# Kernel optimization log

Hardware: AMD Instinct MI355X
Metric: run time of the kernel (lower is better)

## Reference

```python
import jax, jax.numpy as jnp
import numpy as np

HID = 2048 * 3  # infl_ratio = 3
EPS = 1e-5
P_DROP = 0.5


def sign_ste(x):
    # straight-through binarization: sign in fwd, identity in bwd
    return x + jax.lax.stop_gradient(jnp.sign(x) - x)


def batchnorm(x, g, b):
    # training-mode BatchNorm1d: batch stats, biased variance
    m = jnp.mean(x, axis=0)
    v = jnp.mean((x - m) ** 2, axis=0)
    return g * (x - m) / jnp.sqrt(v + EPS) + b


def hardtanh(x):
    return jnp.clip(x, -1.0, 1.0)


def dropout(x, u):
    # u ~ U[0,1); keep where u >= p, scale by 1/(1-p)
    return jnp.where(u >= P_DROP, x / (1.0 - P_DROP), 0.0)


def setup_inputs() -> dict:
    key = jax.random.key(0)
    ks = jax.random.split(key, 16)
    B = 512
    d = {}
    d['x'] = jax.random.normal(ks[0], (B, 784), dtype=jnp.float32)
    d['drop_mask_bin'] = jax.random.uniform(ks[1], (B, HID), dtype=jnp.float32)
    d['drop_mask_real'] = jax.random.uniform(ks[2], (B, HID), dtype=jnp.float32)
    s1 = 1.0 / np.sqrt(784)
    sh = 1.0 / np.sqrt(HID)
    d['w1'] = jax.random.uniform(ks[3], (HID, 784), jnp.float32, -s1, s1)
    d['b1'] = jax.random.uniform(ks[4], (HID,), jnp.float32, -s1, s1)
    d['w2'] = jax.random.uniform(ks[5], (HID, HID), jnp.float32, -sh, sh)
    d['b2'] = jax.random.uniform(ks[6], (HID,), jnp.float32, -sh, sh)
    d['w3'] = jax.random.uniform(ks[7], (HID, HID), jnp.float32, -sh, sh)
    d['b3'] = jax.random.uniform(ks[8], (HID,), jnp.float32, -sh, sh)
    d['w4'] = jax.random.uniform(ks[9], (10, HID), jnp.float32, -sh, sh)
    d['b4'] = jax.random.uniform(ks[10], (10,), jnp.float32, -sh, sh)
    for i, k in zip((1, 2, 3), (ks[11], ks[12], ks[13])):
        d[f'g{i}'] = jnp.ones((HID,), jnp.float32)
        d[f'be{i}'] = jnp.zeros((HID,), jnp.float32)
    return d


def reference(x, drop_mask_bin, drop_mask_real, w1, b1, w2, b2, w3, b3, w4, b4,
              g1, be1, g2, be2, g3, be3):
    sg = jax.lax.stop_gradient
    # layer 1: input dim 784 -> input NOT binarized; weights binarized
    Bout1 = x @ sign_ste(w1).T + b1
    Rout1 = sg(x @ w1.T + b1)
    Bout1 = hardtanh(batchnorm(Bout1, g1, be1))
    Rout1 = sg(hardtanh(batchnorm(Rout1, g1, be1)))
    # layer 2: binarize activations and weights on binary path
    Bout2 = sign_ste(Bout1) @ sign_ste(w2).T + b2
    Rout2 = sg(Rout1 @ w2.T + b2)
    Bout2 = hardtanh(batchnorm(Bout2, g2, be2))
    Rout2 = sg(hardtanh(batchnorm(Rout2, g2, be2)))
    # layer 3 + dropout
    Bout3 = sign_ste(Bout2) @ sign_ste(w3).T + b3
    Rout3 = sg(Rout2 @ w3.T + b3)
    Bout3 = hardtanh(batchnorm(dropout(Bout3, drop_mask_bin), g3, be3))
    Rout3 = sg(hardtanh(batchnorm(dropout(Rout3, drop_mask_real), g3, be3)))
    # classifier (real-valued Linear)
    out = Bout3 @ w4.T + b4
    logp = jax.nn.log_softmax(out, axis=1)
    return (logp, out, Bout1, Rout1, Bout2, Rout2, Bout3, Rout3)
```

## Files before the change

kernel.cpp:

```cpp
#include <hip/hip_runtime.h>


typedef _Float16 f16x8 __attribute__((ext_vector_type(8)));
typedef _Float16 f16x4 __attribute__((ext_vector_type(4)));
typedef float f32x4 __attribute__((ext_vector_type(4)));
typedef int i32x4 __attribute__((ext_vector_type(4)));

#define MFMA16(a, b, c) __builtin_amdgcn_mfma_f32_16x16x32_f16((a), (b), (c), 0, 0, 0)
#define MFMAI8K64(a, b, c) __builtin_amdgcn_mfma_i32_16x16x64_i8((a), (b), (c), 0, 0, 0)

#define HIDC 6144
#define BATCH 512

#define OFF_XH    0ull
#define OFF_Z1LO  851968ull
#define OFF_SB8   13434880ull
#define OFF_RF    16580608ull
#define OFF_STATS 22872064ull
#define OFF_PPART 23068672ull
#define OFF_ZPB   24641536ull
#define OFF_ZPR   37224448ull
#define OFF_ZPR2  49807360ull
#define OFF_ZPR3  62390272ull
#define OFF_W1V   74973184ull
#define OFF_WV    85196800ull
#define OFF_WS8   160694272ull
#define WS_NEED   198443008ull

#define A8_STRIDE 458752ull

__device__ __forceinline__ void load_lds16(const void* g, char* lds) {
  __builtin_amdgcn_global_load_lds((const __attribute__((address_space(1))) void*)g,
                                   (__attribute__((address_space(3))) void*)lds, 16, 0, 0);
}

__global__ __launch_bounds__(256) void k_prep_xq(const float* __restrict__ x,
                                                 char* __restrict__ a8,
                                                 _Float16* __restrict__ xh) {
  int idx = blockIdx.x * 256 + threadIdx.x;
  if (idx >= 512 * 896) return;
  int row = idx / 896, k = idx - row * 896;
  float v = (k < 784) ? x[(size_t)row * 784 + k] : 0.f;
  int q = (int)lrintf(v * 16777216.0f);
  int d0 = ((q + 128) & 255) - 128; q = (q - d0) >> 8;
  int d1 = ((q + 128) & 255) - 128; q = (q - d1) >> 8;
  int d2 = ((q + 128) & 255) - 128; q = (q - d2) >> 8;
  a8[idx] = (char)d0;
  a8[A8_STRIDE + idx] = (char)d1;
  a8[2 * A8_STRIDE + idx] = (char)d2;
  a8[3 * A8_STRIDE + idx] = (char)q;
  if (k < 832) xh[(size_t)row * 832 + k] = (_Float16)v;
}

__global__ __launch_bounds__(256) void k_prep_w1(const float* __restrict__ w,
                                                 char* __restrict__ s1,
                                                 _Float16* __restrict__ w1v) {
  int idx = blockIdx.x * 256 + threadIdx.x;
  if (idx >= 6144 * 896) return;
  int r = idx / 896, k = idx - r * 896;
  float v = (k < 784) ? w[(size_t)r * 784 + k] : 0.f;
  s1[idx] = v > 0.f ? 1 : (v < 0.f ? -1 : 0);
  if (k < 832) w1v[(size_t)r * 832 + k] = (_Float16)v;
}

__global__ __launch_bounds__(256) void k_conv_w23(const float* __restrict__ w,
                                                  _Float16* __restrict__ wv,
                                                  char* __restrict__ ws8) {
  int idx = blockIdx.x * 256 + threadIdx.x;
  size_t o8 = (size_t)idx * 8;
  const float* s = w + o8;
  float4 v0 = *(const float4*)s;
  float4 v1 = *(const float4*)(s + 4);
  float a[8] = {v0.x, v0.y, v0.z, v0.w, v1.x, v1.y, v1.z, v1.w};
  f16x8 hv;
  unsigned long long sbits = 0;
#pragma unroll
  for (int e = 0; e < 8; ++e) {
    hv[e] = (_Float16)a[e];
    char sg = a[e] > 0.f ? 1 : (a[e] < 0.f ? -1 : 0);
    sbits |= ((unsigned long long)(unsigned char)sg) << (8 * e);
  }
  *(f16x8*)(wv + o8) = hv;
  *(unsigned long long*)(ws8 + o8) = sbits;
}

struct MixJob {
  const void* A;
  const void* B;
  float* C;
  int K;
  int kstart;
  int ksteps;
  int is8;
};
struct Mix6 { MixJob j[6]; };

__global__ __launch_bounds__(256) void k_gemm_mix(Mix6 P) {
  __shared__ __align__(16) char smem[65536];
  MixJob J = P.j[0];
  if (blockIdx.z == 1) J = P.j[1];
  if (blockIdx.z == 2) J = P.j[2];
  if (blockIdx.z == 3) J = P.j[3];
  if (blockIdx.z == 4) J = P.j[4];
  if (blockIdx.z == 5) J = P.j[5];
  const int t = threadIdx.x;
  const int lane = t & 63, wid = t >> 6;
  const int wm = wid >> 1, wn = wid & 1;
  const int bn = blockIdx.x, bm = blockIdx.y;
  const size_t K = (size_t)J.K;
  const int nt = J.ksteps;

  if (J.is8) {
    const char* A = (const char*)J.A;
    const char* B = (const char*)J.B;
    i32x4 acc[4][4];
#pragma unroll
    for (int mf = 0; mf < 4; ++mf)
#pragma unroll
      for (int nf = 0; nf < 4; ++nf) acc[mf][nf] = (i32x4){0, 0, 0, 0};

    auto stage = [&](char* dst, int k0) {
#pragma unroll
      for (int i = 0; i < 4; ++i) {
        int p = i * 256 + t;
        int r = p >> 3, c = p & 7;
        int cs = c ^ (r & 7);
        load_lds16(A + (size_t)(bm * 128 + r) * K + k0 + cs * 16, dst + p * 16);
      }
#pragma unroll
      for (int i = 0; i < 4; ++i) {
        int p = i * 256 + t;
        int r = p >> 3, c = p & 7;
        int cs = c ^ (r & 7);
        load_lds16(B + (size_t)(bn * 128 + r) * K + k0 + cs * 16, dst + 16384 + p * 16);
      }
    };

    stage(smem, J.kstart);
    for (int kt = 0; kt < nt; ++kt) {
      char* cbuf = smem + (kt & 1) * 32768;
      char* nbuf = smem + ((kt + 1) & 1) * 32768;
      if (kt + 1 < nt) {
        stage(nbuf, J.kstart + (kt + 1) * 128);
        asm volatile("s_waitcnt vmcnt(8)" ::: "memory");
      } else {
        asm volatile("s_waitcnt vmcnt(0)" ::: "memory");
      }
      __builtin_amdgcn_s_barrier();
      __builtin_amdgcn_s_setprio(1);
#pragma unroll
      for (int kk = 0; kk < 2; ++kk) {
        i32x4 av[4], bv[4];
#pragma unroll
        for (int mf = 0; mf < 4; ++mf) {
          int r = wm * 64 + mf * 16 + (lane & 15);
          int bo = (r * 128 + kk * 64 + (lane >> 4) * 16) ^ ((r & 7) << 4);
          av[mf] = *(const i32x4*)(cbuf + bo);
        }
#pragma unroll
        for (int nf = 0; nf < 4; ++nf) {
          int r = wn * 64 + nf * 16 + (lane & 15);
          int bo = (r * 128 + kk * 64 + (lane >> 4) * 16) ^ ((r & 7) << 4);
          bv[nf] = *(const i32x4*)(cbuf + 16384 + bo);
        }
#pragma unroll
        for (int mf = 0; mf < 4; ++mf)
#pragma unroll
          for (int nf = 0; nf < 4; ++nf) acc[mf][nf] = MFMAI8K64(av[mf], bv[nf], acc[mf][nf]);
      }
      __builtin_amdgcn_s_setprio(0);
      __builtin_amdgcn_s_barrier();
    }
#pragma unroll
    for (int mf = 0; mf < 4; ++mf)
#pragma unroll
      for (int nf = 0; nf < 4; ++nf) {
        int col = bn * 128 + wn * 64 + nf * 16 + (lane & 15);
        int row0 = bm * 128 + wm * 64 + mf * 16 + ((lane >> 4) << 2);
#pragma unroll
        for (int rr = 0; rr < 4; ++rr) {
          J.C[(size_t)(row0 + rr) * HIDC + col] = (float)acc[mf][nf][rr];
        }
      }
  } else {
    const _Float16* A = (const _Float16*)J.A;
    const _Float16* B = (const _Float16*)J.B;
    f32x4 acc[4][4];
#pragma unroll
    for (int mf = 0; mf < 4; ++mf)
#pragma unroll
      for (int nf = 0; nf < 4; ++nf) acc[mf][nf] = (f32x4){0.f, 0.f, 0.f, 0.f};

    auto stage = [&](char* dst, int k0) {
#pragma unroll
      for (int i = 0; i < 4; ++i) {
        int p = i * 256 + t;
        int r = p >> 3, c = p & 7;
        int cs = c ^ (r & 7);
        load_lds16(A + (size_t)(bm * 128 + r) * K + k0 + cs * 8, dst + p * 16);
      }
#pragma unroll
      for (int i = 0; i < 4; ++i) {
        int p = i * 256 + t;
        int r = p >> 3, c = p & 7;
        int cs = c ^ (r & 7);
        load_lds16(B + (size_t)(bn * 128 + r) * K + k0 + cs * 8, dst + 16384 + p * 16);
      }
    };

    stage(smem, J.kstart);
    for (int kt = 0; kt < nt; ++kt) {
      char* cbuf = smem + (kt & 1) * 32768;
      char* nbuf = smem + ((kt + 1) & 1) * 32768;
      if (kt + 1 < nt) {
        stage(nbuf, J.kstart + (kt + 1) * 64);
        asm volatile("s_waitcnt vmcnt(8)" ::: "memory");
      } else {
        asm volatile("s_waitcnt vmcnt(0)" ::: "memory");
      }
      __builtin_amdgcn_s_barrier();
      __builtin_amdgcn_s_setprio(1);
#pragma unroll
      for (int kk = 0; kk < 2; ++kk) {
        f16x8 av[4], bv[4];
#pragma unroll
        for (int mf = 0; mf < 4; ++mf) {
          int r = wm * 64 + mf * 16 + (lane & 15);
          int bo = (r * 128 + kk * 64 + (lane >> 4) * 16) ^ ((r & 7) << 4);
          av[mf] = *(const f16x8*)(cbuf + bo);
        }
#pragma unroll
        for (int nf = 0; nf < 4; ++nf) {
          int r = wn * 64 + nf * 16 + (lane & 15);
          int bo = (r * 128 + kk * 64 + (lane >> 4) * 16) ^ ((r & 7) << 4);
          bv[nf] = *(const f16x8*)(cbuf + 16384 + bo);
        }
#pragma unroll
        for (int mf = 0; mf < 4; ++mf)
#pragma unroll
          for (int nf = 0; nf < 4; ++nf) acc[mf][nf] = MFMA16(av[mf], bv[nf], acc[mf][nf]);
      }
      __builtin_amdgcn_s_setprio(0);
      __builtin_amdgcn_s_barrier();
    }
#pragma unroll
    for (int mf = 0; mf < 4; ++mf)
#pragma unroll
      for (int nf = 0; nf < 4; ++nf) {
        int col = bn * 128 + wn * 64 + nf * 16 + (lane & 15);
        int row0 = bm * 128 + wm * 64 + mf * 16 + ((lane >> 4) << 2);
#pragma unroll
        for (int rr = 0; rr < 4; ++rr) {
          J.C[(size_t)(row0 + rr) * HIDC + col] = acc[mf][nf][rr];
        }
      }
  }
}

struct StJob { const float* Z; const float* Zp0; const float* Zp1; const float* Zp2;
               const float* msk; int digitmode; };
struct St2 { StJob j[2]; const float* bias; int dodrop; double* ppart; };

__global__ __launch_bounds__(256) void k_stats_part(St2 P) {
  __shared__ double sm[4][64];
  __shared__ double sq[4][64];
  const int z = blockIdx.z;
  StJob J = z ? P.j[1] : P.j[0];
  const int li = threadIdx.x & 63, rg = threadIdx.x >> 6;
  const int col = blockIdx.x * 64 + li;
  const double bb = P.dodrop ? (double)P.bias[col] : 0.0;
  double s = 0.0, s2 = 0.0;
#pragma unroll 4
  for (int rr = 0; rr < 16; ++rr) {
    int r = blockIdx.y * 64 + rg * 16 + rr;
    size_t i = (size_t)r * HIDC + col;
    double v;
    if (J.digitmode) {
      double d0 = (double)J.Z[i], d1 = (double)J.Zp0[i];
      double d2 = (double)J.Zp1[i], d3 = (double)J.Zp2[i];
      v = (((d3 * 256.0 + d2) * 256.0 + d1) * 256.0 + d0) * (1.0 / 16777216.0);
    } else {
      v = (double)J.Z[i];
      if (J.Zp0) v += (double)J.Zp0[i];
      if (J.Zp1) v += (double)J.Zp1[i];
      if (J.Zp2) v += (double)J.Zp2[i];
    }
    if (P.dodrop) v = (J.msk[i] >= 0.5f) ? 2.0 * (v + bb) : 0.0;
    s += v;
    s2 += v * v;
  }
  sm[rg][li] = s;
  sq[rg][li] = s2;
  __syncthreads();
  if (rg == 0) {
    double S = sm[0][li] + sm[1][li] + sm[2][li] + sm[3][li];
    double S2 = sq[0][li] + sq[1][li] + sq[2][li] + sq[3][li];
    size_t o = ((size_t)(z * 8 + blockIdx.y) * 2) * HIDC + col;
    P.ppart[o] = S;
    P.ppart[o + HIDC] = S2;
  }
}

__global__ __launch_bounds__(256) void k_stats_fin(const double* __restrict__ ppart,
                                                   double* __restrict__ stats) {
  const int z = blockIdx.z;
  const int c = blockIdx.x * 256 + threadIdx.x;
  double S = 0.0, S2 = 0.0;
#pragma unroll
  for (int y = 0; y < 8; ++y) {
    size_t o = ((size_t)(z * 8 + y) * 2) * HIDC + c;
    S += ppart[o];
    S2 += ppart[o + HIDC];
  }
  double m = S / 512.0;
  double var = S2 / 512.0 - m * m;
  stats[z * 2 * HIDC + c] = m;
  stats[z * 2 * HIDC + HIDC + c] = 1.0 / sqrt(var + 1e-5);
}

struct BnJob { float* Z; const float* Zp0; const float* Zp1; const float* Zp2;
               const float* Zp3; void* aux; const float* msk; int auxmode; int digitmode; };
struct Bn2 {
  BnJob j[2];
  const double* stats;
  const float* g; const float* be; const float* bias;
  int dodrop;
};

__global__ __launch_bounds__(256) void k_bn2(Bn2 P) {
  const int z = blockIdx.z;
  BnJob J = z ? P.j[1] : P.j[0];
  const double* m_arr = P.stats + (size_t)z * 2 * HIDC;
  const double* r_arr = m_arr + HIDC;
  int idx = blockIdx.x * 256 + threadIdx.x;
  int row = idx / 1536;
  int c4 = (idx - row * 1536) * 4;
  size_t base = (size_t)row * HIDC + c4;
  double vv[4];
  if (J.digitmode) {
    float4 d0 = *(const float4*)(J.Zp0 + base);
    float4 d1 = *(const float4*)(J.Zp1 + base);
    float4 d2 = *(const float4*)(J.Zp2 + base);
    float4 d3 = *(const float4*)(J.Zp3 + base);
    const float* p0 = &d0.x;
    const float* p1 = &d1.x;
    const float* p2 = &d2.x;
    const float* p3 = &d3.x;
#pragma unroll
    for (int e = 0; e < 4; ++e)
      vv[e] = ((((double)p3[e] * 256.0 + (double)p2[e]) * 256.0 + (double)p1[e]) * 256.0 +
               (double)p0[e]) * (1.0 / 16777216.0);
  } else {
    float4 zv = *(const float4*)(J.Z + base);
    vv[0] = zv.x; vv[1] = zv.y; vv[2] = zv.z; vv[3] = zv.w;
    if (J.Zp0) {
      float4 t4 = *(const float4*)(J.Zp0 + base);
      vv[0] += t4.x; vv[1] += t4.y; vv[2] += t4.z; vv[3] += t4.w;
    }
    if (J.Zp1) {
      float4 t4 = *(const float4*)(J.Zp1 + base);
      vv[0] += t4.x; vv[1] += t4.y; vv[2] += t4.z; vv[3] += t4.w;
    }
    if (J.Zp2) {
      float4 t4 = *(const float4*)(J.Zp2 + base);
      vv[0] += t4.x; vv[1] += t4.y; vv[2] += t4.z; vv[3] += t4.w;
    }
  }
  float mk[4] = {1.f, 1.f, 1.f, 1.f};
  if (P.dodrop) {
    float4 t4 = *(const float4*)(J.msk + base);
    mk[0] = t4.x; mk[1] = t4.y; mk[2] = t4.z; mk[3] = t4.w;
  }
  float o[4];
  f16x4 a4;
  int sbits = 0;
#pragma unroll
  for (int e = 0; e < 4; ++e) {
    int c = c4 + e;
    double v = vv[e];
    if (P.dodrop) v = (mk[e] >= 0.5f) ? 2.0 * (v + (double)P.bias[c]) : 0.0;
    double bnv = (double)P.g[c] * ((v - m_arr[c]) * r_arr[c]) + (double)P.be[c];
    bnv = bnv > 1.0 ? 1.0 : (bnv < -1.0 ? -1.0 : bnv);
    o[e] = (float)bnv;
    char sg = bnv > 0.0 ? 1 : (bnv < 0.0 ? -1 : 0);
    sbits |= ((int)(unsigned char)sg) << (8 * e);
    a4[e] = (_Float16)o[e];
  }
  float4 ov = {o[0], o[1], o[2], o[3]};
  *(float4*)(J.Z + base) = ov;
  if (J.auxmode == 0) *(int*)((char*)J.aux + base) = sbits;
  if (J.auxmode == 1) *(f16x4*)((_Float16*)J.aux + base) = a4;
}

__global__ __launch_bounds__(256) void k_head(const float* __restrict__ B3,
                                              const float* __restrict__ w4,
                                              const float* __restrict__ b4,
                                              float* __restrict__ out,
                                              float* __restrict__ logp) {
  const int row = blockIdx.x, t = threadIdx.x;
  float acc[10];
#pragma unroll
  for (int j = 0; j < 10; ++j) acc[j] = 0.f;
  const float* a = B3 + (size_t)row * HIDC;
  for (int k4 = t; k4 < 1536; k4 += 256) {
    float4 av = *(const float4*)(a + k4 * 4);
#pragma unroll
    for (int j = 0; j < 10; ++j) {
      float4 wv = *(const float4*)(w4 + (size_t)j * HIDC + k4 * 4);
      acc[j] += av.x * wv.x + av.y * wv.y + av.z * wv.z + av.w * wv.w;
    }
  }
#pragma unroll
  for (int j = 0; j < 10; ++j)
    for (int off = 32; off; off >>= 1) acc[j] += __shfl_down(acc[j], off);
  __shared__ float sred[4][10];
  int wid = t >> 6, ln = t & 63;
  if (ln == 0)
#pragma unroll
    for (int j = 0; j < 10; ++j) sred[wid][j] = acc[j];
  __syncthreads();
  if (t == 0) {
    double o[10];
    double mx = -1e300;
#pragma unroll
    for (int j = 0; j < 10; ++j) {
      o[j] = (double)sred[0][j] + sred[1][j] + sred[2][j] + sred[3][j] + (double)b4[j];
      mx = o[j] > mx ? o[j] : mx;
    }
    double s = 0.0;
#pragma unroll
    for (int j = 0; j < 10; ++j) s += exp(o[j] - mx);
    double l = log(s) + mx;
#pragma unroll
    for (int j = 0; j < 10; ++j) {
      out[row * 10 + j] = (float)o[j];
      logp[row * 10 + j] = (float)(o[j] - l);
    }
  }
}

extern "C" void kernel_launch(void* const* d_in, const int* in_sizes, int n_in,
                              void* d_out, int out_size, void* d_ws, size_t ws_size,
                              hipStream_t stream) {
  const float* x   = (const float*)d_in[0];
  const float* mkb = (const float*)d_in[1];
  const float* mkr = (const float*)d_in[2];
  const float* w1  = (const float*)d_in[3];
  const float* w2  = (const float*)d_in[5];
  const float* w3  = (const float*)d_in[7];
  const float* b3  = (const float*)d_in[8];
  const float* w4  = (const float*)d_in[9];
  const float* b4  = (const float*)d_in[10];
  const float* g1  = (const float*)d_in[11]; const float* be1 = (const float*)d_in[12];
  const float* g2  = (const float*)d_in[13]; const float* be2 = (const float*)d_in[14];
  const float* g3  = (const float*)d_in[15]; const float* be3 = (const float*)d_in[16];

  float* outp = (float*)d_out;
  float* logp = outp;
  float* outo = outp + 5120;
  float* B1 = outp + 10240;
  float* R1 = outp + 3155968;
  float* B2 = outp + 6301696;
  float* R2 = outp + 9447424;
  float* B3 = outp + 12593152;
  float* R3 = outp + 15738880;

  char* ws = (char*)d_ws;
  _Float16* xh  = (_Float16*)(ws + OFF_XH);
  char* sB8     = (char*)(ws + OFF_SB8);
  _Float16* rF  = (_Float16*)(ws + OFF_RF);
  double* stats = (double*)(ws + OFF_STATS);
  double* ppart = (double*)(ws + OFF_PPART);
  float* zpb    = (float*)(ws + OFF_ZPB);
  float* zpr    = (float*)(ws + OFF_ZPR);
  float* zpr2   = (float*)(ws + OFF_ZPR2);
  float* zpr3   = (float*)(ws + OFF_ZPR3);
  _Float16* w1v = (_Float16*)(ws + OFF_W1V);
  _Float16* wv  = (_Float16*)(ws + OFF_WV);
  char* ws8     = (char*)(ws + OFF_WS8);
  char* a8 = (char*)(ws + OFF_WS8);
  char* s1 = (char*)(ws + OFF_WS8 + 4ull * A8_STRIDE);

  k_prep_xq<<<1792, 256, 0, stream>>>(x, a8, xh);
  k_prep_w1<<<21504, 256, 0, stream>>>(w1, s1, w1v);
  {
    Mix6 P{};
    P.j[0] = {a8,                 s1, zpb,  896, 0, 7, 1};
    P.j[1] = {a8 + A8_STRIDE,     s1, zpr,  896, 0, 7, 1};
    P.j[2] = {a8 + 2 * A8_STRIDE, s1, zpr2, 896, 0, 7, 1};
    P.j[3] = {a8 + 3 * A8_STRIDE, s1, zpr3, 896, 0, 7, 1};
    P.j[4] = {xh, w1v, R1, 832, 0, 13, 0};
    P.j[5] = P.j[4];
    k_gemm_mix<<<dim3(48, 4, 5), 256, 0, stream>>>(P);
  }
  {
    St2 S{};
    S.j[0] = {zpb, zpr, zpr2, zpr3, nullptr, 1};
    S.j[1] = {R1, nullptr, nullptr, nullptr, nullptr, 0};
    S.bias = nullptr; S.dodrop = 0; S.ppart = ppart;
    k_stats_part<<<dim3(96, 8, 2), 256, 0, stream>>>(S);
    k_stats_fin<<<dim3(24, 1, 2), 256, 0, stream>>>(ppart, stats);
    Bn2 B{};
    B.j[0] = {B1, zpb, zpr, zpr2, zpr3, sB8, nullptr, 0, 1};
    B.j[1] = {R1, nullptr, nullptr, nullptr, nullptr, rF, nullptr, 1, 0};
    B.stats = stats; B.g = g1; B.be = be1; B.bias = nullptr; B.dodrop = 0;
    k_bn2<<<dim3(3072, 1, 2), 256, 0, stream>>>(B);
  }
  k_conv_w23<<<18432, 256, 0, stream>>>(w2, wv, ws8);
  {
    Mix6 P{};
    P.j[0] = {sB8, ws8, B2,  HIDC, 0,    24, 1};
    P.j[1] = {sB8, ws8, zpb, HIDC, 3072, 24, 1};
    P.j[2] = {rF,  wv,  R2,  HIDC, 0,    48, 0};
    P.j[3] = {rF,  wv,  zpr, HIDC, 3072, 48, 0};
    k_gemm_mix<<<dim3(48, 4, 4), 256, 0, stream>>>(P);
  }
  {
    St2 S{};
    S.j[0] = {B2, zpb, nullptr, nullptr, nullptr, 0};
    S.j[1] = {R2, zpr, nullptr, nullptr, nullptr, 0};
    S.bias = nullptr; S.dodrop = 0; S.ppart = ppart;
    k_stats_part<<<dim3(96, 8, 2), 256, 0, stream>>>(S);
    k_stats_fin<<<dim3(24, 1, 2), 256, 0, stream>>>(ppart, stats);
    Bn2 B{};
    B.j[0] = {B2, zpb, nullptr, nullptr, nullptr, sB8, nullptr, 0, 0};
    B.j[1] = {R2, zpr, nullptr, nullptr, nullptr, rF, nullptr, 1, 0};
    B.stats = stats; B.g = g2; B.be = be2; B.bias = nullptr; B.dodrop = 0;
    k_bn2<<<dim3(3072, 1, 2), 256, 0, stream>>>(B);
  }
  k_conv_w23<<<18432, 256, 0, stream>>>(w3, wv, ws8);
  {
    Mix6 P{};
    P.j[0] = {sB8, ws8, B3,  HIDC, 0,    24, 1};
    P.j[1] = {sB8, ws8, zpb, HIDC, 3072, 24, 1};
    P.j[2] = {rF,  wv,  R3,  HIDC, 0,    48, 0};
    P.j[3] = {rF,  wv,  zpr, HIDC, 3072, 48, 0};
    k_gemm_mix<<<dim3(48, 4, 4), 256, 0, stream>>>(P);
  }
  {
    St2 S{};
    S.j[0] = {B3, zpb, nullptr, nullptr, mkb, 0};
    S.j[1] = {R3, zpr, nullptr, nullptr, mkr, 0};
    S.bias = b3; S.dodrop = 1; S.ppart = ppart;
    k_stats_part<<<dim3(96, 8, 2), 256, 0, stream>>>(S);
    k_stats_fin<<<dim3(24, 1, 2), 256, 0, stream>>>(ppart, stats);
    Bn2 B{};
    B.j[0] = {B3, zpb, nullptr, nullptr, nullptr, nullptr, mkb, 2, 0};
    B.j[1] = {R3, zpr, nullptr, nullptr, nullptr, nullptr, mkr, 2, 0};
    B.stats = stats; B.g = g3; B.be = be3; B.bias = b3; B.dodrop = 1;
    k_bn2<<<dim3(3072, 1, 2), 256, 0, stream>>>(B);
  }
  k_head<<<512, 256, 0, stream>>>(B3, w4, b4, outo, logp);
}
```

Before: 460.4 us.

## Fold weight conversions into neighboring kernels as extra grid slices

The two input-prep kernels are merged into one launch. The standalone w2/w3 fp16 and sign conversion kernels are removed and their work is added as extra blockIdx.z slices. The w2 conversion now runs inside the layer-1 GEMM launch, and the w3 conversion is split between the layer-2 stats and BN launches. The a8/s1 buffers move to a separate workspace region so they no longer alias ws8 while w2 is being written concurrently. This cuts kernel launches and lets conversion bandwidth overlap with compute-bound GEMM and BN work, at the cost of uneven per-block work inside the shared grids.

```diff
diff --git a/kernel.cpp b/kernel.cpp
--- a/kernel.cpp
+++ b/kernel.cpp
@@ -13,7 +13,7 @@
 #define BATCH 512
 
 #define OFF_XH    0ull
-#define OFF_Z1LO  851968ull
+#define OFF_A8S1  851968ull
 #define OFF_SB8   13434880ull
 #define OFF_RF    16580608ull
 #define OFF_STATS 22872064ull
@@ -34,43 +34,11 @@
                                    (__attribute__((address_space(3))) void*)lds, 16, 0, 0);
 }
 
-__global__ __launch_bounds__(256) void k_prep_xq(const float* __restrict__ x,
-                                                 char* __restrict__ a8,
-                                                 _Float16* __restrict__ xh) {
-  int idx = blockIdx.x * 256 + threadIdx.x;
-  if (idx >= 512 * 896) return;
-  int row = idx / 896, k = idx - row * 896;
-  float v = (k < 784) ? x[(size_t)row * 784 + k] : 0.f;
-  int q = (int)lrintf(v * 16777216.0f);
-  int d0 = ((q + 128) & 255) - 128; q = (q - d0) >> 8;
-  int d1 = ((q + 128) & 255) - 128; q = (q - d1) >> 8;
-  int d2 = ((q + 128) & 255) - 128; q = (q - d2) >> 8;
-  a8[idx] = (char)d0;
-  a8[A8_STRIDE + idx] = (char)d1;
-  a8[2 * A8_STRIDE + idx] = (char)d2;
-  a8[3 * A8_STRIDE + idx] = (char)q;
-  if (k < 832) xh[(size_t)row * 832 + k] = (_Float16)v;
-}
-
-__global__ __launch_bounds__(256) void k_prep_w1(const float* __restrict__ w,
-                                                 char* __restrict__ s1,
-                                                 _Float16* __restrict__ w1v) {
-  int idx = blockIdx.x * 256 + threadIdx.x;
-  if (idx >= 6144 * 896) return;
-  int r = idx / 896, k = idx - r * 896;
-  float v = (k < 784) ? w[(size_t)r * 784 + k] : 0.f;
-  s1[idx] = v > 0.f ? 1 : (v < 0.f ? -1 : 0);
-  if (k < 832) w1v[(size_t)r * 832 + k] = (_Float16)v;
-}
-
-__global__ __launch_bounds__(256) void k_conv_w23(const float* __restrict__ w,
-                                                  _Float16* __restrict__ wv,
-                                                  char* __restrict__ ws8) {
-  int idx = blockIdx.x * 256 + threadIdx.x;
-  size_t o8 = (size_t)idx * 8;
-  const float* s = w + o8;
-  float4 v0 = *(const float4*)s;
-  float4 v1 = *(const float4*)(s + 4);
+__device__ __forceinline__ void conv8(const float* __restrict__ s,
+                                      _Float16* __restrict__ wv,
+                                      char* __restrict__ s8, size_t o8) {
+  float4 v0 = *(const float4*)(s + o8);
+  float4 v1 = *(const float4*)(s + o8 + 4);
   float a[8] = {v0.x, v0.y, v0.z, v0.w, v1.x, v1.y, v1.z, v1.w};
   f16x8 hv;
   unsigned long long sbits = 0;
@@ -81,7 +49,37 @@
     sbits |= ((unsigned long long)(unsigned char)sg) << (8 * e);
   }
   *(f16x8*)(wv + o8) = hv;
-  *(unsigned long long*)(ws8 + o8) = sbits;
+  *(unsigned long long*)(s8 + o8) = sbits;
+}
+
+__global__ __launch_bounds__(256) void k_prep_all(const float* __restrict__ x,
+                                                  const float* __restrict__ w,
+                                                  char* __restrict__ a8,
+                                                  _Float16* __restrict__ xh,
+                                                  char* __restrict__ s1,
+                                                  _Float16* __restrict__ w1v) {
+  if (blockIdx.x < 1792) {
+    int idx = blockIdx.x * 256 + threadIdx.x;
+    if (idx >= 512 * 896) return;
+    int row = idx / 896, k = idx - row * 896;
+    float v = (k < 784) ? x[(size_t)row * 784 + k] : 0.f;
+    int q = (int)lrintf(v * 16777216.0f);
+    int d0 = ((q + 128) & 255) - 128; q = (q - d0) >> 8;
+    int d1 = ((q + 128) & 255) - 128; q = (q - d1) >> 8;
+    int d2 = ((q + 128) & 255) - 128; q = (q - d2) >> 8;
+    a8[idx] = (char)d0;
+    a8[A8_STRIDE + idx] = (char)d1;
+    a8[2 * A8_STRIDE + idx] = (char)d2;
+    a8[3 * A8_STRIDE + idx] = (char)q;
+    if (k < 832) xh[(size_t)row * 832 + k] = (_Float16)v;
+  } else {
+    int idx = (blockIdx.x - 1792) * 256 + threadIdx.x;
+    if (idx >= 6144 * 896) return;
+    int r = idx / 896, k = idx - r * 896;
+    float v = (k < 784) ? w[(size_t)r * 784 + k] : 0.f;
+    s1[idx] = v > 0.f ? 1 : (v < 0.f ? -1 : 0);
+    if (k < 832) w1v[(size_t)r * 832 + k] = (_Float16)v;
+  }
 }
 
 struct MixJob {
@@ -110,7 +108,19 @@
   const size_t K = (size_t)J.K;
   const int nt = J.ksteps;
 
-  if (J.is8) {
+  if (J.is8 == 2) {
+    const float* srcw = (const float*)J.A;
+    _Float16* wvo = (_Float16*)J.B;
+    char* s8o = (char*)J.C;
+    int bid = bm * 48 + bn;
+    for (int i = 0; i < 96; ++i) {
+      size_t g8 = ((size_t)bid * 96 + i) * 256 + t;
+      conv8(srcw, wvo, s8o, g8 * 8);
+    }
+    return;
+  }
+
+  if (J.is8 == 1) {
     const char* A = (const char*)J.A;
     const char* B = (const char*)J.B;
     i32x4 acc[4][4];
@@ -259,12 +269,21 @@
 
 struct StJob { const float* Z; const float* Zp0; const float* Zp1; const float* Zp2;
                const float* msk; int digitmode; };
-struct St2 { StJob j[2]; const float* bias; int dodrop; double* ppart; };
+struct St2 { StJob j[2]; const float* bias; int dodrop; double* ppart;
+             const float* wsrc; _Float16* wvdst; char* s8dst; };
 
 __global__ __launch_bounds__(256) void k_stats_part(St2 P) {
+  const int z = blockIdx.z;
+  if (z == 2) {
+    int bid = blockIdx.y * 96 + blockIdx.x;
+    for (int i = 0; i < 12; ++i) {
+      size_t g8 = ((size_t)bid * 12 + i) * 256 + threadIdx.x;
+      conv8(P.wsrc, P.wvdst, P.s8dst, g8 * 8);
+    }
+    return;
+  }
   __shared__ double sm[4][64];
   __shared__ double sq[4][64];
-  const int z = blockIdx.z;
   StJob J = z ? P.j[1] : P.j[0];
   const int li = threadIdx.x & 63, rg = threadIdx.x >> 6;
   const int col = blockIdx.x * 64 + li;
@@ -325,10 +344,19 @@
   const double* stats;
   const float* g; const float* be; const float* bias;
   int dodrop;
+  const float* wsrc; _Float16* wvdst; char* s8dst;
 };
 
 __global__ __launch_bounds__(256) void k_bn2(Bn2 P) {
   const int z = blockIdx.z;
+  if (z == 2) {
+    int bid = blockIdx.x;
+    for (int i = 0; i < 3; ++i) {
+      size_t g8 = 2359296ull + ((size_t)bid * 3 + i) * 256 + threadIdx.x;
+      conv8(P.wsrc, P.wvdst, P.s8dst, g8 * 8);
+    }
+    return;
+  }
   BnJob J = z ? P.j[1] : P.j[0];
   const double* m_arr = P.stats + (size_t)z * 2 * HIDC;
   const double* r_arr = m_arr + HIDC;
@@ -467,6 +495,8 @@
 
   char* ws = (char*)d_ws;
   _Float16* xh  = (_Float16*)(ws + OFF_XH);
+  char* a8      = (char*)(ws + OFF_A8S1);
+  char* s1      = (char*)(ws + OFF_A8S1 + 4ull * A8_STRIDE);
   char* sB8     = (char*)(ws + OFF_SB8);
   _Float16* rF  = (_Float16*)(ws + OFF_RF);
   double* stats = (double*)(ws + OFF_STATS);
@@ -478,11 +508,8 @@
   _Float16* w1v = (_Float16*)(ws + OFF_W1V);
   _Float16* wv  = (_Float16*)(ws + OFF_WV);
   char* ws8     = (char*)(ws + OFF_WS8);
-  char* a8 = (char*)(ws + OFF_WS8);
-  char* s1 = (char*)(ws + OFF_WS8 + 4ull * A8_STRIDE);
-
-  k_prep_xq<<<1792, 256, 0, stream>>>(x, a8, xh);
-  k_prep_w1<<<21504, 256, 0, stream>>>(w1, s1, w1v);
+
+  k_prep_all<<<23296, 256, 0, stream>>>(x, w1, a8, xh, s1, w1v);
   {
     Mix6 P{};
     P.j[0] = {a8,                 s1, zpb,  896, 0, 7, 1};
@@ -490,8 +517,8 @@
     P.j[2] = {a8 + 2 * A8_STRIDE, s1, zpr2, 896, 0, 7, 1};
     P.j[3] = {a8 + 3 * A8_STRIDE, s1, zpr3, 896, 0, 7, 1};
     P.j[4] = {xh, w1v, R1, 832, 0, 13, 0};
-    P.j[5] = P.j[4];
-    k_gemm_mix<<<dim3(48, 4, 5), 256, 0, stream>>>(P);
+    P.j[5] = {w2, wv, (float*)ws8, 0, 0, 0, 2};
+    k_gemm_mix<<<dim3(48, 4, 6), 256, 0, stream>>>(P);
   }
   {
     St2 S{};
@@ -506,7 +533,6 @@
     B.stats = stats; B.g = g1; B.be = be1; B.bias = nullptr; B.dodrop = 0;
     k_bn2<<<dim3(3072, 1, 2), 256, 0, stream>>>(B);
   }
-  k_conv_w23<<<18432, 256, 0, stream>>>(w2, wv, ws8);
   {
     Mix6 P{};
     P.j[0] = {sB8, ws8, B2,  HIDC, 0,    24, 1};
@@ -520,15 +546,16 @@
     S.j[0] = {B2, zpb, nullptr, nullptr, nullptr, 0};
     S.j[1] = {R2, zpr, nullptr, nullptr, nullptr, 0};
     S.bias = nullptr; S.dodrop = 0; S.ppart = ppart;
-    k_stats_part<<<dim3(96, 8, 2), 256, 0, stream>>>(S);
+    S.wsrc = w3; S.wvdst = wv; S.s8dst = ws8;
+    k_stats_part<<<dim3(96, 8, 3), 256, 0, stream>>>(S);
     k_stats_fin<<<dim3(24, 1, 2), 256, 0, stream>>>(ppart, stats);
     Bn2 B{};
     B.j[0] = {B2, zpb, nullptr, nullptr, nullptr, sB8, nullptr, 0, 0};
     B.j[1] = {R2, zpr, nullptr, nullptr, nullptr, rF, nullptr, 1, 0};
     B.stats = stats; B.g = g2; B.be = be2; B.bias = nullptr; B.dodrop = 0;
-    k_bn2<<<dim3(3072, 1, 2), 256, 0, stream>>>(B);
-  }
-  k_conv_w23<<<18432, 256, 0, stream>>>(w3, wv, ws8);
+    B.wsrc = w3; B.wvdst = wv; B.s8dst = ws8;
+    k_bn2<<<dim3(3072, 1, 3), 256, 0, stream>>>(B);
+  }
   {
     Mix6 P{};
     P.j[0] = {sB8, ws8, B3,  HIDC, 0,    24, 1};
```

After: 496.7 us. 7.9% more time.
